# Optimization experiments

Measured on AMD Instinct MI355X. Metric: run time of the kernel, lower is better.

The kernel has to match this reference:

```python
import jax, jax.numpy as jnp
import numpy as np

EPS = 1e-5  # BatchNorm1d default eps


def _gcn(h_in, W, b, src, dst, dinv):
    h = h_in @ W  # [N, D]
    coef = dinv[src] * dinv[dst]  # [E]
    agg = jax.ops.segment_sum(h[src] * coef[:, None], dst, num_segments=h.shape[0])
    agg = agg + h * (dinv * dinv)[:, None]  # self-loop contribution
    return agg + b


def _bn(h, gamma, beta):
    # training-mode BatchNorm1d over the node dimension (biased variance)
    mu = jnp.mean(h, axis=0)
    var = jnp.var(h, axis=0)
    return gamma * (h - mu) * jax.lax.rsqrt(var + EPS) + beta


def setup_inputs() -> dict:
    key = jax.random.key(0)
    N, E, F_IN, D, B = 50000, 800000, 64, 256, 1000
    ks = jax.random.split(key, 8)
    x = jax.random.normal(ks[0], (N, F_IN), dtype=jnp.float32)
    edge_index = jax.random.randint(ks[1], (2, E), 0, N)
    batch_index = (jnp.arange(N) * B) // N  # sorted, every graph non-empty (~50 nodes each)
    s = lambda k, sh: (jax.random.normal(k, sh, dtype=jnp.float32) * 0.05)
    inp = {
        "x": x, "edge_index": edge_index, "batch_index": batch_index, "num_graphs": B,
        "W0": s(ks[2], (F_IN, D)), "b0": jnp.zeros((D,), jnp.float32),
        "W1": s(ks[3], (D, D)), "b1": jnp.zeros((D,), jnp.float32),
        "W2": s(ks[4], (D, D)), "b2": jnp.zeros((D,), jnp.float32),
        "W3": s(ks[5], (D, D)), "b3": jnp.zeros((D,), jnp.float32),
        "g0": jnp.ones((D,), jnp.float32), "be0": jnp.zeros((D,), jnp.float32),
        "g1": jnp.ones((D,), jnp.float32), "be1": jnp.zeros((D,), jnp.float32),
        "g2": jnp.ones((D,), jnp.float32), "be2": jnp.zeros((D,), jnp.float32),
        "g3": jnp.ones((D,), jnp.float32), "be3": jnp.zeros((D,), jnp.float32),
        "Wout": s(ks[6], (2 * D, 1)), "bout": jnp.zeros((1,), jnp.float32),
    }
    return inp


def reference(x, edge_index, batch_index, num_graphs,
              W0, b0, W1, b1, W2, b2, W3, b3,
              g0, be0, g1, be1, g2, be2, g3, be3,
              Wout, bout):
    N = x.shape[0]
    src, dst = edge_index[0], edge_index[1]
    # degree after adding self-loops (all edge weights = 1)
    deg = 1.0 + jax.ops.segment_sum(jnp.ones(src.shape[0], x.dtype), dst, num_segments=N)
    dinv = jax.lax.rsqrt(deg)

    h = x
    for W, b, g, be in ((W0, b0, g0, be0), (W1, b1, g1, be1),
                        (W2, b2, g2, be2), (W3, b3, g3, be3)):
        h = jnp.tanh(_bn(_gcn(h, W, b, src, dst, dinv), g, be))

    # global max pool + global average pool over graphs
    hmax = jax.ops.segment_max(h, batch_index, num_segments=num_graphs)
    hsum = jax.ops.segment_sum(h, batch_index, num_segments=num_graphs)
    cnt = jax.ops.segment_sum(jnp.ones(N, x.dtype), batch_index, num_segments=num_graphs)
    hmean = hsum / cnt[:, None]
    hidden = jnp.concatenate([hmax, hmean], axis=1)  # [B, 512]
    out = hidden @ Wout + bout  # [B, 1]
    return (out, hidden)
```

## Files before the change

kernel.cpp:

```cpp
#include <hip/hip_runtime.h>
#include <hip/hip_bf16.h>
#include <math.h>

#define D 256
#define EPS 1e-5f
#define SCAN_NB 256

typedef _Float16 f16;
typedef _Float16 f16x4 __attribute__((ext_vector_type(4)));
typedef _Float16 f16x8 __attribute__((ext_vector_type(8)));
typedef float f32x4v __attribute__((ext_vector_type(4)));
typedef unsigned int uint;

__device__ __forceinline__ float fast_tanh(float x) {
    float e = __expf(2.f * x);
    return 1.f - __fdividef(2.f, e + 1.f);
}

union HU { f16 h; unsigned short u; };
__device__ __forceinline__ uint pack_rec(int s, float c) {
    HU hu; hu.h = (f16)c;
    return ((uint)s << 16) | (uint)hu.u;
}
__device__ __forceinline__ float rec_coef(uint r) {
    HU hu; hu.u = (unsigned short)(r & 0xffffu);
    return (float)hu.h;
}

__device__ __forceinline__ void cp16(f16* lds, const f16* g) {
    __builtin_amdgcn_global_load_lds(
        (const __attribute__((address_space(1))) unsigned int*)g,
        (__attribute__((address_space(3))) unsigned int*)lds, 16, 0, 0);
}

__global__ void k_count(const int* __restrict__ dst, int* __restrict__ cnt,
                        int* __restrict__ rank, int E) {
    int e = blockIdx.x * blockDim.x + threadIdx.x;
    if (e < E) rank[e] = atomicAdd(&cnt[dst[e]], 1);
}

__global__ void k_scan_part(const int* __restrict__ cnt, int* __restrict__ row_ptr,
                            int* __restrict__ partial, int N, int C) {
    __shared__ int sdata[256];
    int b = blockIdx.x, t = threadIdx.x;
    int base = b * C;
    int end = base + C; if (end > N) end = N;
    int running = 0;
    for (int ts = base; ts < end; ts += 256) {
        int idx = ts + t;
        int val = (idx < end) ? cnt[idx] : 0;
        sdata[t] = val;
        __syncthreads();
        for (int s = 1; s < 256; s <<= 1) {
            int v = (t >= s) ? sdata[t - s] : 0;
            __syncthreads();
            sdata[t] += v;
            __syncthreads();
        }
        if (idx < end) row_ptr[idx] = running + sdata[t] - val;
        running += sdata[255];
        __syncthreads();
    }
    if (t == 0) partial[b] = running;
}

__global__ void k_scan_off(int* __restrict__ partial) {
    __shared__ int sdata[256];
    int t = threadIdx.x;
    int val = partial[t];
    sdata[t] = val;
    __syncthreads();
    for (int s = 1; s < 256; s <<= 1) {
        int v = (t >= s) ? sdata[t - s] : 0;
        __syncthreads();
        sdata[t] += v;
        __syncthreads();
    }
    partial[t] = sdata[t] - val;
}

__global__ void k_scan_add(int* __restrict__ row_ptr,
                           const int* __restrict__ partial, const int* __restrict__ cnt,
                           float* __restrict__ dinv, int N, int C, int E) {
    int i = blockIdx.x * 256 + threadIdx.x;
    if (i < N) {
        row_ptr[i] += partial[i / C];
        dinv[i] = rsqrtf(1.0f + (float)cnt[i]);
    }
    if (i == N) row_ptr[N] = E;
}

__global__ void k_fill(const int* __restrict__ src, const int* __restrict__ dst,
                       const int* __restrict__ rank, const int* __restrict__ row_ptr,
                       const float* __restrict__ dinv, uint* __restrict__ ecp, int E) {
    int e = blockIdx.x * blockDim.x + threadIdx.x;
    if (e >= E) return;
    int s = src[e], t = dst[e];
    ecp[row_ptr[t] + rank[e]] = pack_rec(s, dinv[s] * dinv[t]);
}

__global__ void k_cast(const float* __restrict__ in, f16* __restrict__ o, int n4,
                       float* __restrict__ sums, float* __restrict__ sumsq) {
    int i = blockIdx.x * 256 + threadIdx.x;
    if (blockIdx.x == 0) {
        sums[threadIdx.x]  = 0.f;
        sumsq[threadIdx.x] = 0.f;
    }
    if (i >= n4) return;
    float4 v = ((const float4*)in)[i];
    f16x4 h = {(f16)v.x, (f16)v.y, (f16)v.z, (f16)v.w};
    ((f16x4*)o)[i] = h;
}

__global__ void k_prep_w_all(const float* __restrict__ W0, const float* __restrict__ W1,
                             const float* __restrict__ W2, const float* __restrict__ W3,
                             f16* __restrict__ T0, f16* __restrict__ T1,
                             f16* __restrict__ T2, f16* __restrict__ T3) {
    int idx = blockIdx.x * 256 + threadIdx.x;
    if (idx < 16384) {
        int k = idx >> 8, d = idx & 255;
        T0[(size_t)d * 64 + k] = (f16)W0[idx];
        return;
    }
    idx -= 16384;
    const float* W; f16* T;
    if (idx < 65536)      { W = W1; T = T1; }
    else if (idx < 131072){ W = W2; T = T2; idx -= 65536; }
    else                  { W = W3; T = T3; idx -= 131072; }
    int k = idx >> 8, d = idx & 255;
    T[(size_t)d * 256 + k] = (f16)W[idx];
}

#define KSTEP 64
__global__ __launch_bounds__(256)
void k_gemm(const f16* __restrict__ A, const f16* __restrict__ Wt,
            f16* __restrict__ outh, int K,
            float* __restrict__ sums, float* __restrict__ sumsq) {
    __shared__ __align__(16) f16 As[128 * 64];
    __shared__ __align__(16) f16 Bs[128 * 64];
    const int r0 = blockIdx.x * 128;
    const int c0 = blockIdx.y * 128;
    const int t = threadIdx.x;
    const int lane = t & 63, wave = t >> 6;
    const int wr = wave >> 1, wc = wave & 1;
    const int quad = lane >> 4, m = lane & 15;

    f32x4v acc[4][4];
#pragma unroll
    for (int i = 0; i < 4; ++i)
#pragma unroll
        for (int j = 0; j < 4; ++j) acc[i][j] = {0.f, 0.f, 0.f, 0.f};

    int aoff[4], boff[4], loff[4];
#pragma unroll
    for (int u = 0; u < 4; ++u) {
        int idx = u * 256 + t;
        int row = idx >> 3;
        int s   = (idx & 7) ^ (row & 7);
        aoff[u] = (r0 + row) * K + s * 8;
        boff[u] = (c0 + row) * K + s * 8;
        loff[u] = (u * 256 + (t & ~63)) * 8;
    }

    for (int k0 = 0; k0 < K; k0 += KSTEP) {
#pragma unroll
        for (int u = 0; u < 4; ++u)
            cp16(As + loff[u], A + (size_t)aoff[u] + k0);
#pragma unroll
        for (int u = 0; u < 4; ++u)
            cp16(Bs + loff[u], Wt + (size_t)boff[u] + k0);
        __syncthreads();

#pragma unroll
        for (int kk = 0; kk < 2; ++kk) {
            f16x8 af[4], bf[4];
#pragma unroll
            for (int i = 0; i < 4; ++i) {
                int row = wr * 64 + i * 16 + m;
                int s   = (kk * 4 + quad) ^ (row & 7);
                af[i] = *(const f16x8*)((const char*)As + row * 128 + (s << 4));
            }
#pragma unroll
            for (int j = 0; j < 4; ++j) {
                int row = wc * 64 + j * 16 + m;
                int s   = (kk * 4 + quad) ^ (row & 7);
                bf[j] = *(const f16x8*)((const char*)Bs + row * 128 + (s << 4));
            }
#pragma unroll
            for (int i = 0; i < 4; ++i)
#pragma unroll
                for (int j = 0; j < 4; ++j)
                    acc[i][j] = __builtin_amdgcn_mfma_f32_16x16x32_f16(af[i], bf[j], acc[i][j], 0, 0, 0);
        }
        __syncthreads();
    }

#pragma unroll
    for (int i = 0; i < 4; ++i) {
#pragma unroll
        for (int r = 0; r < 4; ++r) {
            int row = r0 + wr * 64 + i * 16 + quad * 4 + r;
#pragma unroll
            for (int j = 0; j < 4; ++j) {
                int colm = c0 + wc * 64 + j * 16 + m;
                outh[(size_t)row * D + colm] = (f16)acc[i][j][r];
            }
        }
    }

    {
        __shared__ float cs[128], css[128];
        if (t < 128) { cs[t] = 0.f; css[t] = 0.f; }
        __syncthreads();
#pragma unroll
        for (int j = 0; j < 4; ++j) {
            int f = wc * 64 + j * 16 + m;
            float s = 0.f, q = 0.f;
#pragma unroll
            for (int i = 0; i < 4; ++i)
#pragma unroll
                for (int r = 0; r < 4; ++r) {
                    float v = acc[i][j][r];
                    s += v; q += v * v;
                }
            atomicAdd(&cs[f], s);
            atomicAdd(&css[f], q);
        }
        __syncthreads();
        if (t < 128) {
            atomicAdd(&sums[c0 + t], cs[t]);
            atomicAdd(&sumsq[c0 + t], css[t]);
        }
    }
}

__global__ __launch_bounds__(256)
void k_gather_q(const int* __restrict__ row_ptr, const uint4* __restrict__ ecp4,
                const unsigned char* __restrict__ hq, const float* __restrict__ dinv,
                f16* __restrict__ out, float* __restrict__ sums,
                float* __restrict__ sumsq, float* __restrict__ scf_out,
                const float* __restrict__ scf_in, int N) {
    sums[threadIdx.x]  = 0.f;
    sumsq[threadIdx.x] = 0.f;

    const int lane = threadIdx.x & 63;
    const int wave = threadIdx.x >> 6;
    const uint* __restrict__ hqu = (const uint*)hq;
    f16x4* __restrict__ out4 = (f16x4*)out;

    const int wtotal = gridDim.x * 4;
    int i = blockIdx.x * 4 + wave;
    if (i >= N) return;

    int lo = row_ptr[i], hi = row_ptr[i + 1];
    float dv = dinv[i];
    float sci = scf_in ? scf_in[i] : 0.f;
    uint selfu = hqu[(uint)i * 64u + (uint)lane];

    while (true) {
        int inext = i + wtotal;
        int lo2 = 0, hi2 = 0; float dv2 = 0.f, sci2 = 0.f; uint su2 = 0u;
        if (inext < N) {
            lo2 = row_ptr[inext]; hi2 = row_ptr[inext + 1];
            dv2 = dinv[inext];
            if (scf_in) sci2 = scf_in[inext];
            su2 = hqu[(uint)inext * 64u + (uint)lane];
        }

        float dd = dv * dv;
        float scf = scf_in ? sci : dd;
        float4 acc;
        acc.x = (float)(selfu & 0xffu) * dd;
        acc.y = (float)((selfu >> 8) & 0xffu) * dd;
        acc.z = (float)((selfu >> 16) & 0xffu) * dd;
        acc.w = (float)(selfu >> 24) * dd;

        for (int e = (lo & ~3); e < hi; e += 8) {
            uint4 p0 = ecp4[(e >> 2)];
            uint4 p1 = ecp4[(e >> 2) + 1];
            uint pr[8] = {p0.x, p0.y, p0.z, p0.w, p1.x, p1.y, p1.z, p1.w};
            uint rv[8]; float cf[8];
            if ((e >= lo) & (e + 8 <= hi)) {
#pragma unroll
                for (int j = 0; j < 8; ++j) {
                    uint rec = __builtin_amdgcn_readfirstlane(pr[j]);
                    const uint* rp = hqu + ((rec >> 16) << 6);
                    rv[j] = rp[lane];
                    cf[j] = rec_coef(rec);
                }
            } else {
#pragma unroll
                for (int j = 0; j < 8; ++j) {
                    int ej = e + j;
                    bool v = (ej >= lo) & (ej < hi);
                    uint rec = __builtin_amdgcn_readfirstlane(pr[j]);
                    const uint* rp = hqu + ((rec >> 16) << 6);
                    rv[j] = rp[lane];
                    cf[j] = v ? rec_coef(rec) : 0.f;
                }
            }
#pragma unroll
            for (int j = 0; j < 8; ++j) {
                float c = cf[j];
                uint v = rv[j];
                acc.x = fmaf((float)(v & 0xffu), c, acc.x);
                acc.y = fmaf((float)((v >> 8) & 0xffu), c, acc.y);
                acc.z = fmaf((float)((v >> 16) & 0xffu), c, acc.z);
                acc.w = fmaf((float)(v >> 24), c, acc.w);
            }
            if (!scf_in) {
#pragma unroll
                for (int j = 0; j < 8; ++j) scf += cf[j];
            }
        }

        acc.x = fmaf(-128.f, scf, acc.x);
        acc.y = fmaf(-128.f, scf, acc.y);
        acc.z = fmaf(-128.f, scf, acc.z);
        acc.w = fmaf(-128.f, scf, acc.w);

        f16x4 o = {(f16)acc.x, (f16)acc.y, (f16)acc.z, (f16)acc.w};
        out4[(uint)i * 64u + (uint)lane] = o;
        if (scf_out && lane == 0) scf_out[i] = scf;

        if (inext >= N) break;
        i = inext; lo = lo2; hi = hi2; dv = dv2; sci = sci2; selfu = su2;
    }
}

__global__ __launch_bounds__(256)
void k_gather64(const int* __restrict__ row_ptr, const uint4* __restrict__ ecp4,
                const f16* __restrict__ xh, const float* __restrict__ dinv,
                f16* __restrict__ aggx, int N) {
    const int lane = threadIdx.x & 63;
    const int wave = threadIdx.x >> 6;
    const int q = lane >> 4, m = lane & 15;
    const f16x4* __restrict__ x4 = (const f16x4*)xh;
    f16x4* __restrict__ o4 = (f16x4*)aggx;

    int slot   = blockIdx.x * 4 + wave;
    int stride = gridDim.x * 4;
    for (int i0 = slot * 4; i0 < N; i0 += stride * 4) {
        int i = i0 + q;
        bool act = i < N;
        int ii = act ? i : 0;
        int lo = act ? row_ptr[ii] : 0;
        int hi = act ? row_ptr[ii + 1] : 0;
        float dd = act ? dinv[ii] : 0.f; dd *= dd;
        f16x4 hv = act ? x4[(uint)ii * 16u + (uint)m] : (f16x4){0, 0, 0, 0};
        float4 acc;
        acc.x = (float)hv[0] * dd; acc.y = (float)hv[1] * dd;
        acc.z = (float)hv[2] * dd; acc.w = (float)hv[3] * dd;

        for (int e = (lo & ~3); e < hi; e += 8) {
            uint4 p0 = ecp4[(e >> 2)];
            uint4 p1 = ecp4[(e >> 2) + 1];
            uint pr[8] = {p0.x, p0.y, p0.z, p0.w, p1.x, p1.y, p1.z, p1.w};
            int nd[8]; float cf[8];
#pragma unroll
            for (int j = 0; j < 8; ++j) {
                int ej = e + j;
                bool v = (ej >= lo) & (ej < hi);
                nd[j] = v ? (int)(pr[j] >> 16) : ii;
                cf[j] = v ? rec_coef(pr[j]) : 0.f;
            }
            f16x4 r[8];
#pragma unroll
            for (int j = 0; j < 8; ++j) r[j] = x4[(uint)nd[j] * 16u + (uint)m];
#pragma unroll
            for (int j = 0; j < 8; ++j) {
                acc.x = fmaf((float)r[j][0], cf[j], acc.x);
                acc.y = fmaf((float)r[j][1], cf[j], acc.y);
                acc.z = fmaf((float)r[j][2], cf[j], acc.z);
                acc.w = fmaf((float)r[j][3], cf[j], acc.w);
            }
        }
        if (act) {
            f16x4 o = {(f16)acc.x, (f16)acc.y, (f16)acc.z, (f16)acc.w};
            o4[(uint)i * 16u + (uint)m] = o;
        }
    }
}

__global__ __launch_bounds__(256)
void k_bn_tanh_q(const f16* __restrict__ h, const float* __restrict__ sums,
                 const float* __restrict__ sumsq, const float* __restrict__ g,
                 const float* __restrict__ be, float Ninv,
                 unsigned char* __restrict__ hq, int N) {
    const int t = threadIdx.x;
    const int d0 = (t & 31) * 8;
    const int rs = t >> 5;

    float s[8], sh[8];
#pragma unroll
    for (int j = 0; j < 8; ++j) {
        float mu  = sums[d0 + j] * Ninv;
        float var = sumsq[d0 + j] * Ninv - mu * mu;
        float sc  = g[d0 + j] * rsqrtf(var + EPS);
        s[j]  = sc;
        sh[j] = be[d0 + j] - mu * sc;
    }

    const int rstride = gridDim.x * 8;
    for (int r = blockIdx.x * 8 + rs; r < N; r += rstride) {
        f16x8 v = *(const f16x8*)(h + (size_t)r * D + d0);
        uint b[8];
#pragma unroll
        for (int j = 0; j < 8; ++j) {
            float tv = fast_tanh(fmaf((float)v[j], s[j], sh[j]));
            b[j] = (uint)(__float2int_rn(tv * 127.f) + 128);
        }
        uint2 o;
        o.x = b[0] | (b[1] << 8) | (b[2] << 16) | (b[3] << 24);
        o.y = b[4] | (b[5] << 8) | (b[6] << 16) | (b[7] << 24);
        *(uint2*)(hq + (size_t)r * D + d0) = o;
    }
}

__device__ __forceinline__ int lb(const int* __restrict__ a, int n, int v) {
    int lo = 0, hi = n;
    while (lo < hi) {
        int mid = (lo + hi) >> 1;
        if (a[mid] < v) lo = mid + 1; else hi = mid;
    }
    return lo;
}

__global__ void k_pool(const f16* __restrict__ hw, const float* __restrict__ sums,
                       const float* __restrict__ sumsq, const float* __restrict__ gg,
                       const float* __restrict__ be, float Ninv,
                       const int* __restrict__ batch,
                       const float* __restrict__ Wout, const float* __restrict__ bout,
                       float* __restrict__ out, float* __restrict__ hidden, int N) {
    int g = blockIdx.x;
    int d = threadIdx.x;
    float mu  = sums[d] * Ninv;
    float var = sumsq[d] * Ninv - mu * mu;
    float sc  = gg[d] * rsqrtf(var + EPS);
    float sh  = be[d] - mu * sc;

    int lo = lb(batch, N, g);
    int hi = lb(batch, N, g + 1);
    float mx = -INFINITY, sm = 0.0f;
    for (int i = lo; i < hi; ++i) {
        float v = fast_tanh(fmaf((float)hw[(size_t)i * D + d], sc, sh));
        mx = fmaxf(mx, v);
        sm += v;
    }
    float mean = sm / (float)(hi - lo);
    hidden[(size_t)g * (2 * D) + d] = mx;
    hidden[(size_t)g * (2 * D) + D + d] = mean;

    float p = mx * Wout[d] + mean * Wout[D + d];
    __shared__ float red[256];
    red[d] = p;
    __syncthreads();
    for (int s = 128; s > 0; s >>= 1) {
        if (d < s) red[d] += red[d + s];
        __syncthreads();
    }
    if (d == 0) out[g] = red[0] + bout[0];
}

extern "C" void kernel_launch(void* const* d_in, const int* in_sizes, int n_in,
                              void* d_out, int out_size, void* d_ws, size_t ws_size,
                              hipStream_t stream) {
    const float* x          = (const float*)d_in[0];
    const int*   edge_index = (const int*)d_in[1];
    const int*   batch      = (const int*)d_in[2];
    const float* Wl[4] = {(const float*)d_in[4], (const float*)d_in[6],
                          (const float*)d_in[8], (const float*)d_in[10]};
    const float* gl[4]  = {(const float*)d_in[12], (const float*)d_in[14],
                           (const float*)d_in[16], (const float*)d_in[18]};
    const float* bel[4] = {(const float*)d_in[13], (const float*)d_in[15],
                           (const float*)d_in[17], (const float*)d_in[19]};
    const float* Wout = (const float*)d_in[20];
    const float* bout = (const float*)d_in[21];

    const int N = in_sizes[0] / 64;
    const int E = in_sizes[1] / 2;
    const int B = out_size / (1 + 2 * D);
    const int NB   = (N + 127) / 128;
    const int NPAD = NB * 128;

    const int* srcv = edge_index;
    const int* dstv = edge_index + E;

    f16*   hw_h    = (f16*)d_ws;
    f16*   hh      = hw_h + (size_t)NPAD * D;
    f16*   agg_h   = hh + (size_t)N * D;
    f16*   xh      = agg_h + (size_t)NPAD * D;
    f16*   aggx    = xh + (size_t)N * 64;
    f16*   Wt0     = aggx + (size_t)NPAD * 64;
    f16*   Wt1     = Wt0 + 256 * 64;
    f16*   Wt2     = Wt1 + 256 * 256;
    f16*   Wt3     = Wt2 + 256 * 256;
    float* dinv    = (float*)(Wt3 + 256 * 256);
    float* sums    = dinv + N;
    float* sumsq   = sums + D;
    float* scfs    = sumsq + D;
    uint*  ecp     = (uint*)(scfs + N);
    int*   rank    = (int*)(ecp + E + 16);
    int*   cnt     = rank + E;
    int*   row_ptr = cnt + N;
    int*   partial = row_ptr + N + 1;

    unsigned char* hq = (unsigned char*)hh;
    const uint4* ecp4 = (const uint4*)ecp;

    float* out_p    = (float*)d_out;
    float* hidden_p = out_p + B;

    hipMemsetAsync(cnt, 0, (size_t)N * sizeof(int), stream);
    hipMemsetAsync(agg_h + (size_t)N * D, 0, (size_t)(NPAD - N) * D * sizeof(f16), stream);
    hipMemsetAsync(aggx + (size_t)N * 64, 0, (size_t)(NPAD - N) * 64 * sizeof(f16), stream);
    k_count<<<(E + 255) / 256, 256, 0, stream>>>(dstv, cnt, rank, E);
    const int C = (N + SCAN_NB - 1) / SCAN_NB;
    k_scan_part<<<SCAN_NB, 256, 0, stream>>>(cnt, row_ptr, partial, N, C);
    k_scan_off<<<1, 256, 0, stream>>>(partial);
    k_scan_add<<<(N + 1 + 255) / 256, 256, 0, stream>>>(row_ptr, partial,
                                                        cnt, dinv, N, C, E);
    k_fill<<<(E + 255) / 256, 256, 0, stream>>>(srcv, dstv, rank, row_ptr,
                                                dinv, ecp, E);

    k_cast<<<(N * 64 / 4 + 255) / 256, 256, 0, stream>>>(x, xh, N * 64 / 4, sums, sumsq);
    k_prep_w_all<<<(16384 + 3 * 65536 + 255) / 256, 256, 0, stream>>>(
        Wl[0], Wl[1], Wl[2], Wl[3], Wt0, Wt1, Wt2, Wt3);

    const dim3 gemm_grid(NB, 2);
    const float Ninv = 1.0f / (float)N;
    const int bn_grid = (N + 7) / 8;
    f16* Wts[4] = {Wt0, Wt1, Wt2, Wt3};

    k_gather64<<<2048, 256, 0, stream>>>(row_ptr, ecp4, xh, dinv, aggx, N);
    k_gemm<<<gemm_grid, 256, 0, stream>>>(aggx, Wt0, hw_h, 64, sums, sumsq);
    k_bn_tanh_q<<<bn_grid, 256, 0, stream>>>(
        hw_h, sums, sumsq, gl[0], bel[0], Ninv, hq, N);

    for (int l = 1; l < 4; ++l) {
        k_gather_q<<<4096, 256, 0, stream>>>(row_ptr, ecp4, hq, dinv,
                                             agg_h, sums, sumsq,
                                             (l == 1) ? scfs : nullptr,
                                             (l > 1) ? scfs : nullptr, N);
        k_gemm<<<gemm_grid, 256, 0, stream>>>(agg_h, Wts[l], hw_h, 256,
                                              sums, sumsq);
        if (l < 3) {
            k_bn_tanh_q<<<bn_grid, 256, 0, stream>>>(
                hw_h, sums, sumsq, gl[l], bel[l], Ninv, hq, N);
        }
    }

    k_pool<<<B, 256, 0, stream>>>(hw_h, sums, sumsq, gl[3], bel[3], Ninv,
                                  batch, Wout, bout, out_p, hidden_p, N);
}
```

Before: 507.0 us.

## Split degree counters four ways and swizzle GEMM blocks across XCDs

The degree-count atomics now target four replicated counters per node (picked by edge index mod 4), which cuts contention on popular destination nodes. The scan, dinv and fill kernels sum or prefix the four counters to recover the CSR offsets. Separately, the GEMM grid is flattened to 1D and remapped so that consecutive tiles land on the same XCD, which keeps the row and column tiles sharing an A tile on one die for better L2 reuse. The cost is four times the counter memory and extra int4 reads in the scan and fill kernels.

```diff
diff --git a/kernel.cpp b/kernel.cpp
--- a/kernel.cpp
+++ b/kernel.cpp
@@ -33,22 +33,24 @@
         (__attribute__((address_space(3))) unsigned int*)lds, 16, 0, 0);
 }
 
-__global__ void k_count(const int* __restrict__ dst, int* __restrict__ cnt,
+__global__ void k_count(const int* __restrict__ dst, int* __restrict__ cnt4,
                         int* __restrict__ rank, int E) {
     int e = blockIdx.x * blockDim.x + threadIdx.x;
-    if (e < E) rank[e] = atomicAdd(&cnt[dst[e]], 1);
-}
-
-__global__ void k_scan_part(const int* __restrict__ cnt, int* __restrict__ row_ptr,
+    if (e < E) rank[e] = atomicAdd(&cnt4[(dst[e] << 2) | (e & 3)], 1);
+}
+
+__global__ void k_scan_part(const int* __restrict__ cnt4, int* __restrict__ row_ptr,
                             int* __restrict__ partial, int N, int C) {
     __shared__ int sdata[256];
+    const int4* __restrict__ c4 = (const int4*)cnt4;
     int b = blockIdx.x, t = threadIdx.x;
     int base = b * C;
     int end = base + C; if (end > N) end = N;
     int running = 0;
     for (int ts = base; ts < end; ts += 256) {
         int idx = ts + t;
-        int val = (idx < end) ? cnt[idx] : 0;
+        int val = 0;
+        if (idx < end) { int4 c = c4[idx]; val = c.x + c.y + c.z + c.w; }
         sdata[t] = val;
         __syncthreads();
         for (int s = 1; s < 256; s <<= 1) {
@@ -80,23 +82,28 @@
 }
 
 __global__ void k_scan_add(int* __restrict__ row_ptr,
-                           const int* __restrict__ partial, const int* __restrict__ cnt,
+                           const int* __restrict__ partial, const int* __restrict__ cnt4,
                            float* __restrict__ dinv, int N, int C, int E) {
     int i = blockIdx.x * 256 + threadIdx.x;
     if (i < N) {
         row_ptr[i] += partial[i / C];
-        dinv[i] = rsqrtf(1.0f + (float)cnt[i]);
+        int4 c = ((const int4*)cnt4)[i];
+        dinv[i] = rsqrtf(1.0f + (float)(c.x + c.y + c.z + c.w));
     }
     if (i == N) row_ptr[N] = E;
 }
 
 __global__ void k_fill(const int* __restrict__ src, const int* __restrict__ dst,
                        const int* __restrict__ rank, const int* __restrict__ row_ptr,
+                       const int* __restrict__ cnt4,
                        const float* __restrict__ dinv, uint* __restrict__ ecp, int E) {
     int e = blockIdx.x * blockDim.x + threadIdx.x;
     if (e >= E) return;
     int s = src[e], t = dst[e];
-    ecp[row_ptr[t] + rank[e]] = pack_rec(s, dinv[s] * dinv[t]);
+    int4 c = ((const int4*)cnt4)[t];
+    int rep = e & 3;
+    int pre = ((rep > 0) ? c.x : 0) + ((rep > 1) ? c.y : 0) + ((rep > 2) ? c.z : 0);
+    ecp[row_ptr[t] + pre + rank[e]] = pack_rec(s, dinv[s] * dinv[t]);
 }
 
 __global__ void k_cast(const float* __restrict__ in, f16* __restrict__ o, int n4,
@@ -138,8 +145,12 @@
             float* __restrict__ sums, float* __restrict__ sumsq) {
     __shared__ __align__(16) f16 As[128 * 64];
     __shared__ __align__(16) f16 Bs[128 * 64];
-    const int r0 = blockIdx.x * 128;
-    const int c0 = blockIdx.y * 128;
+    const int total = gridDim.x;
+    const int q = total >> 3, r = total & 7;
+    const int xcd = blockIdx.x & 7, j = blockIdx.x >> 3;
+    const int swz = (xcd < r ? xcd * (q + 1) : r * (q + 1) + (xcd - r) * q) + j;
+    const int c0 = (swz & 1) * 128;
+    const int r0 = (swz >> 1) * 128;
     const int t = threadIdx.x;
     const int lane = t & 63, wave = t >> 6;
     const int wr = wave >> 1, wc = wave & 1;
@@ -149,7 +160,7 @@
 #pragma unroll
     for (int i = 0; i < 4; ++i)
 #pragma unroll
-        for (int j = 0; j < 4; ++j) acc[i][j] = {0.f, 0.f, 0.f, 0.f};
+        for (int j2 = 0; j2 < 4; ++j2) acc[i][j2] = {0.f, 0.f, 0.f, 0.f};
 
     int aoff[4], boff[4], loff[4];
 #pragma unroll
@@ -181,16 +192,16 @@
                 af[i] = *(const f16x8*)((const char*)As + row * 128 + (s << 4));
             }
 #pragma unroll
-            for (int j = 0; j < 4; ++j) {
-                int row = wc * 64 + j * 16 + m;
+            for (int j2 = 0; j2 < 4; ++j2) {
+                int row = wc * 64 + j2 * 16 + m;
                 int s   = (kk * 4 + quad) ^ (row & 7);
-                bf[j] = *(const f16x8*)((const char*)Bs + row * 128 + (s << 4));
+                bf[j2] = *(const f16x8*)((const char*)Bs + row * 128 + (s << 4));
             }
 #pragma unroll
             for (int i = 0; i < 4; ++i)
 #pragma unroll
-                for (int j = 0; j < 4; ++j)
-                    acc[i][j] = __builtin_amdgcn_mfma_f32_16x16x32_f16(af[i], bf[j], acc[i][j], 0, 0, 0);
+                for (int j2 = 0; j2 < 4; ++j2)
+                    acc[i][j2] = __builtin_amdgcn_mfma_f32_16x16x32_f16(af[i], bf[j2], acc[i][j2], 0, 0, 0);
         }
         __syncthreads();
     }
@@ -198,12 +209,12 @@
 #pragma unroll
     for (int i = 0; i < 4; ++i) {
 #pragma unroll
-        for (int r = 0; r < 4; ++r) {
-            int row = r0 + wr * 64 + i * 16 + quad * 4 + r;
-#pragma unroll
-            for (int j = 0; j < 4; ++j) {
-                int colm = c0 + wc * 64 + j * 16 + m;
-                outh[(size_t)row * D + colm] = (f16)acc[i][j][r];
+        for (int r2 = 0; r2 < 4; ++r2) {
+            int row = r0 + wr * 64 + i * 16 + quad * 4 + r2;
+#pragma unroll
+            for (int j2 = 0; j2 < 4; ++j2) {
+                int colm = c0 + wc * 64 + j2 * 16 + m;
+                outh[(size_t)row * D + colm] = (f16)acc[i][j2][r2];
             }
         }
     }
@@ -213,18 +224,18 @@
         if (t < 128) { cs[t] = 0.f; css[t] = 0.f; }
         __syncthreads();
 #pragma unroll
-        for (int j = 0; j < 4; ++j) {
-            int f = wc * 64 + j * 16 + m;
-            float s = 0.f, q = 0.f;
+        for (int j2 = 0; j2 < 4; ++j2) {
+            int f = wc * 64 + j2 * 16 + m;
+            float s = 0.f, qq = 0.f;
 #pragma unroll
             for (int i = 0; i < 4; ++i)
 #pragma unroll
-                for (int r = 0; r < 4; ++r) {
-                    float v = acc[i][j][r];
-                    s += v; q += v * v;
+                for (int r2 = 0; r2 < 4; ++r2) {
+                    float v = acc[i][j2][r2];
+                    s += v; qq += v * v;
                 }
             atomicAdd(&cs[f], s);
-            atomicAdd(&css[f], q);
+            atomicAdd(&css[f], qq);
         }
         __syncthreads();
         if (t < 128) {
@@ -501,8 +512,8 @@
     float* scfs    = sumsq + D;
     uint*  ecp     = (uint*)(scfs + N);
     int*   rank    = (int*)(ecp + E + 16);
-    int*   cnt     = rank + E;
-    int*   row_ptr = cnt + N;
+    int*   cnt4    = rank + E;
+    int*   row_ptr = cnt4 + 4 * N;
     int*   partial = row_ptr + N + 1;
 
     unsigned char* hq = (unsigned char*)hh;
@@ -511,23 +522,23 @@
     float* out_p    = (float*)d_out;
     float* hidden_p = out_p + B;
 
-    hipMemsetAsync(cnt, 0, (size_t)N * sizeof(int), stream);
+    hipMemsetAsync(cnt4, 0, (size_t)4 * N * sizeof(int), stream);
     hipMemsetAsync(agg_h + (size_t)N * D, 0, (size_t)(NPAD - N) * D * sizeof(f16), stream);
     hipMemsetAsync(aggx + (size_t)N * 64, 0, (size_t)(NPAD - N) * 64 * sizeof(f16), stream);
-    k_count<<<(E + 255) / 256, 256, 0, stream>>>(dstv, cnt, rank, E);
+    k_count<<<(E + 255) / 256, 256, 0, stream>>>(dstv, cnt4, rank, E);
     const int C = (N + SCAN_NB - 1) / SCAN_NB;
-    k_scan_part<<<SCAN_NB, 256, 0, stream>>>(cnt, row_ptr, partial, N, C);
+    k_scan_part<<<SCAN_NB, 256, 0, stream>>>(cnt4, row_ptr, partial, N, C);
     k_scan_off<<<1, 256, 0, stream>>>(partial);
     k_scan_add<<<(N + 1 + 255) / 256, 256, 0, stream>>>(row_ptr, partial,
-                                                        cnt, dinv, N, C, E);
+                                                        cnt4, dinv, N, C, E);
     k_fill<<<(E + 255) / 256, 256, 0, stream>>>(srcv, dstv, rank, row_ptr,
-                                                dinv, ecp, E);
+                                                cnt4, dinv, ecp, E);
 
     k_cast<<<(N * 64 / 4 + 255) / 256, 256, 0, stream>>>(x, xh, N * 64 / 4, sums, sumsq);
     k_prep_w_all<<<(16384 + 3 * 65536 + 255) / 256, 256, 0, stream>>>(
         Wl[0], Wl[1], Wl[2], Wl[3], Wt0, Wt1, Wt2, Wt3);
 
-    const dim3 gemm_grid(NB, 2);
+    const int gemm_grid = NB * 2;
     const float Ninv = 1.0f / (float)N;
     const int bn_grid = (N + 7) / 8;
     f16* Wts[4] = {Wt0, Wt1, Wt2, Wt3};
```

After: 506.3 us. Within noise of the previous version (-0.1%).
